# Kernel tuning notes

Hardware: AMD Instinct MI355X
Metric: run time of the kernel (lower is better)

## Reference

```python
import jax, jax.numpy as jnp
import numpy as np


def _conv3x3(x, w, b):
    # NCHW conv, stride 1, pad 1
    y = jax.lax.conv_general_dilated(x, w, (1, 1), ((1, 1), (1, 1)),
                                     dimension_numbers=('NCHW', 'OIHW', 'NCHW'))
    return y + b[None, :, None, None]


def _deform_conv3x3(x, offset, w):
    # Deformable conv v1: 3x3, stride 1, pad 1, 1 deformable group, no bias.
    # offset: [B, 18, H, W] laid out as (dy_k, dx_k) for k = 0..8 (row-major taps).
    B, C, H, W = x.shape
    K = 9
    off = offset.reshape(B, K, 2, H, W)
    ky, kx = jnp.meshgrid(jnp.arange(3), jnp.arange(3), indexing='ij')
    ky = (ky.reshape(K) - 1).astype(x.dtype)  # kernel tap y-offset, pad=1
    kx = (kx.reshape(K) - 1).astype(x.dtype)
    hh = jnp.arange(H, dtype=x.dtype)
    ww = jnp.arange(W, dtype=x.dtype)
    # sampling locations [B, K, H, W]
    sy = hh[None, None, :, None] + ky[None, :, None, None] + off[:, :, 0]
    sx = ww[None, None, None, :] + kx[None, :, None, None] + off[:, :, 1]
    y0 = jnp.floor(sy)
    x0 = jnp.floor(sx)
    ly = sy - y0  # fractional parts
    lx = sx - x0
    x_flat = x.reshape(B, C, H * W)

    def gather(yi, xi, wgt):
        # zero-padding semantics: corners outside the image contribute 0
        valid = (yi >= 0) & (yi < H) & (xi >= 0) & (xi < W)
        idx = (jnp.clip(yi, 0, H - 1).astype(jnp.int32) * W
               + jnp.clip(xi, 0, W - 1).astype(jnp.int32)).reshape(B, 1, K * H * W)
        v = jnp.take_along_axis(x_flat, idx, axis=2).reshape(B, C, K, H, W)
        return v * (wgt * valid.astype(x.dtype))[:, None]

    sampled = (gather(y0,     x0,     (1 - ly) * (1 - lx))
             + gather(y0,     x0 + 1, (1 - ly) * lx)
             + gather(y0 + 1, x0,     ly * (1 - lx))
             + gather(y0 + 1, x0 + 1, ly * lx))  # [B, C, K, H, W]
    return jnp.einsum('bckhw,ock->bohw', sampled, w.reshape(w.shape[0], C, K))


def setup_inputs() -> dict:
    key = jax.random.key(0)
    ks = jax.random.split(key, 8)
    C, O = 256, 256
    return {
        'kernel': jax.random.normal(ks[0], (16, C, 16, 16), jnp.float32),
        'search': jax.random.normal(ks[1], (16, C, 32, 32), jnp.float32),
        'Toffset_w': jax.random.normal(ks[2], (18, C, 3, 3), jnp.float32) * 0.02,
        'Toffset_b': jnp.zeros((18,), jnp.float32),
        'Tdeform_w': jax.random.normal(ks[3], (O, C, 3, 3), jnp.float32) * 0.02,
        'Soffset_w': jax.random.normal(ks[4], (18, C, 3, 3), jnp.float32) * 0.02,
        'Soffset_b': jnp.zeros((18,), jnp.float32),
        'Sdeform_w': jax.random.normal(ks[5], (O, C, 3, 3), jnp.float32) * 0.02,
    }


def reference(kernel, search, Toffset_w, Toffset_b, Tdeform_w,
              Soffset_w, Soffset_b, Sdeform_w):
    kernel_offset = _conv3x3(kernel, Toffset_w, Toffset_b)
    kernel_out = _deform_conv3x3(kernel, kernel_offset, Tdeform_w)
    search_offset = _conv3x3(search, Soffset_w, Soffset_b)
    search_out = _deform_conv3x3(search, search_offset, Sdeform_w)
    return (kernel_out, search_out, kernel_offset, search_offset)
```

## Files before the change

kernel.cpp:

```cpp
#include <hip/hip_runtime.h>

#define CIN   256
#define OC    256
#define K_TOT 2304
#define CCH   32
#define NCHK  8
#define KCH   288
#define SSTR  296
#define DM    64

#define N_DW  (OC * K_TOT)
#define N_OW  (32 * K_TOT)
#define N_CVT (2 * N_DW + 2 * N_OW)
#define CVT_BLOCKS (N_CVT / 4 / 256)

typedef short  bf16x8 __attribute__((ext_vector_type(8)));
typedef float  f32x4  __attribute__((ext_vector_type(4)));
typedef unsigned short ushort_t;

__device__ __forceinline__ ushort_t f2bf(float f) {
    unsigned u = __builtin_bit_cast(unsigned, f);
    u += 0x7fffu + ((u >> 16) & 1u);
    return (ushort_t)(u >> 16);
}
__device__ __forceinline__ float bf2f(short s) {
    return __builtin_bit_cast(float, ((unsigned)(unsigned short)s) << 16);
}

__global__ __launch_bounds__(256) void prep_k(
    const float* __restrict__ tdw, const float* __restrict__ sdw,
    const float* __restrict__ tow, const float* __restrict__ sow,
    const float* __restrict__ kin, const float* __restrict__ sin_,
    ushort_t* __restrict__ wk_d, ushort_t* __restrict__ ws_d,
    ushort_t* __restrict__ wk_o, ushort_t* __restrict__ ws_o,
    ushort_t* __restrict__ xt_k, ushort_t* __restrict__ xt_s)
{
    __shared__ ushort_t tile[64][264];

    if (blockIdx.x < CVT_BLOCKS) {
        const int i = (blockIdx.x * 256 + threadIdx.x) * 4;
        const float* src; ushort_t* dst; int j; bool offw = false;
        if (i < N_DW)                    { src = tdw; dst = wk_d; j = i; }
        else if (i < 2 * N_DW)           { src = sdw; dst = ws_d; j = i - N_DW; }
        else if (i < 2 * N_DW + N_OW)    { src = tow; dst = wk_o; j = i - 2 * N_DW; offw = true; }
        else                             { src = sow; dst = ws_o; j = i - 2 * N_DW - N_OW; offw = true; }
        const int oc = j / K_TOT;
        const int k  = j - oc * K_TOT;
        const int cc = k / KCH;
        const int r  = k - cc * KCH;
        const int tap = r >> 5;
        const int cl  = r & 31;
        ushort4 o4 = {0, 0, 0, 0};
        if (!offw || oc < 18) {
            const float* sp = &src[((size_t)oc * CIN + cc * 32 + cl) * 9 + tap];
            o4.x = f2bf(sp[0]); o4.y = f2bf(sp[9]); o4.z = f2bf(sp[18]); o4.w = f2bf(sp[27]);
        }
        *(ushort4*)&dst[j] = o4;
        return;
    }

    const int bx2 = blockIdx.x - CVT_BLOCKS;
    int H, W, b, px0; const float* x; ushort_t* xt;
    if (bx2 < 64) {
        H = 16; W = 16; x = kin; xt = xt_k;
        b = bx2 >> 2; px0 = (bx2 & 3) * 64;
    } else {
        int t2 = bx2 - 64;
        H = 32; W = 32; x = sin_; xt = xt_s;
        b = t2 >> 4; px0 = (t2 & 15) * 64;
    }
    const int HW = H * W;
    const int t = threadIdx.x, lane = t & 63, wv = t >> 6;
    const float* xb = x + (size_t)b * CIN * HW;

    for (int it = 0; it < 16; ++it) {
        const int ch = wv * 64 + it * 4 + (lane >> 4);
        const int pq = (lane & 15) * 4;
        float4 v = *(const float4*)&xb[(size_t)ch * HW + px0 + pq];
        tile[pq + 0][ch] = f2bf(v.x);
        tile[pq + 1][ch] = f2bf(v.y);
        tile[pq + 2][ch] = f2bf(v.z);
        tile[pq + 3][ch] = f2bf(v.w);
    }
    __syncthreads();
    for (int it = 0; it < 8; ++it) {
        const int px = it * 8 + wv * 2 + (lane >> 5);
        const int cg = (lane & 31) * 8;
        bf16x8 v = *(const bf16x8*)&tile[px][cg];
        *(bf16x8*)&xt[((size_t)b * HW + px0 + px) * 256 + cg] = v;
    }
}

__global__ __launch_bounds__(512, 2) void conv_gemm_k(
    const ushort_t* __restrict__ xt_k, const ushort_t* __restrict__ kwgt,
    const float* __restrict__ kbias, float* __restrict__ kout,
    const ushort_t* __restrict__ xt_s, const ushort_t* __restrict__ swgt,
    const float* __restrict__ sbias, float* __restrict__ sout)
{
    __shared__ float sred[3][4][2][64][4];

    int H, W, sh, b, px0;
    const ushort_t* xt; const ushort_t* wgt; const float* bias; float* out;
    if (blockIdx.x < 64) {
        H = 16; W = 16; sh = 4; xt = xt_k; wgt = kwgt; bias = kbias; out = kout;
        b = blockIdx.x >> 2; px0 = (blockIdx.x & 3) * 64;
    } else {
        int t2 = blockIdx.x - 64;
        H = 32; W = 32; sh = 5; xt = xt_s; wgt = swgt; bias = sbias; out = sout;
        b = t2 >> 4; px0 = (t2 & 15) * 64;
    }
    const int HW = H * W;
    const int t = threadIdx.x, lane = t & 63, wv = t >> 6;
    const int kh = wv >> 1;
    const int nt = wv & 1;
    const int l15 = lane & 15;
    const int cg8 = (lane >> 4) * 8;
    const ushort_t* xtb = xt + (size_t)b * HW * 256;

    int h[4], wc[4];
#pragma unroll
    for (int mt = 0; mt < 4; ++mt) {
        const int px = px0 + mt * 16 + l15;
        h[mt]  = px >> sh;
        wc[mt] = px & (W - 1);
    }
    const ushort_t* wrow = wgt + (size_t)(nt * 16 + l15) * K_TOT + cg8;

    f32x4 acc[4] = {};
    for (int cc = kh * 2; cc < kh * 2 + 2; ++cc) {
        const int cb = cc * 32 + cg8;
#pragma unroll
        for (int ks = 0; ks < 9; ++ks) {
            const bf16x8 b0 = *(const bf16x8*)&wrow[(size_t)cc * KCH + ks * 32];
            const int dy = ks / 3 - 1, dx = ks % 3 - 1;
#pragma unroll
            for (int mt = 0; mt < 4; ++mt) {
                const int y  = h[mt] + dy;
                const int xx = wc[mt] + dx;
                const bool ok = ((unsigned)y < (unsigned)H) && ((unsigned)xx < (unsigned)W);
                bf16x8 a = {};
                if (ok) a = *(const bf16x8*)&xtb[(size_t)(((y << sh) + xx) * 256 + cb)];
                acc[mt] = __builtin_amdgcn_mfma_f32_16x16x32_bf16(a, b0, acc[mt], 0, 0, 0);
            }
        }
    }

    if (kh > 0) {
#pragma unroll
        for (int mt = 0; mt < 4; ++mt)
            *(float4*)&sred[kh - 1][mt][nt][lane][0] = *(float4*)&acc[mt];
    }
    __syncthreads();
    if (kh == 0) {
        const int oc = nt * 16 + l15;
        const int prow = (lane >> 4) * 4;
        if (oc < 18) {
            const float bs = bias[oc];
#pragma unroll
            for (int mt = 0; mt < 4; ++mt) {
                float4 r = *(float4*)&acc[mt];
#pragma unroll
                for (int q = 0; q < 3; ++q) {
                    const float4 o = *(const float4*)&sred[q][mt][nt][lane][0];
                    r.x += o.x; r.y += o.y; r.z += o.z; r.w += o.w;
                }
                r.x += bs; r.y += bs; r.z += bs; r.w += bs;
                *(float4*)(out + ((size_t)b * 18 + oc) * HW + px0 + mt * 16 + prow) = r;
            }
        }
    }
}

__device__ __forceinline__ void dcn_load4(
    bf16x8* c, const ushort_t* __restrict__ xtb, int4 id, int cb)
{
    c[0] = *(const bf16x8*)&xtb[(size_t)id.x * 256 + cb];
    c[1] = *(const bf16x8*)&xtb[(size_t)id.y * 256 + cb];
    c[2] = *(const bf16x8*)&xtb[(size_t)id.z * 256 + cb];
    c[3] = *(const bf16x8*)&xtb[(size_t)id.w * 256 + cb];
}
__device__ __forceinline__ void dcn_proc2(
    ushort_t* swb, int so, const bf16x8* c, float4 wt)
{
    bf16x8 r;
#pragma unroll
    for (int j = 0; j < 8; ++j) {
        const float v = wt.x * bf2f(c[0][j]) + wt.y * bf2f(c[1][j])
                      + wt.z * bf2f(c[2][j]) + wt.w * bf2f(c[3][j]);
        r[j] = (short)f2bf(v);
    }
    *(bf16x8*)&swb[so] = r;
}

__global__ __launch_bounds__(512, 4) void deform_gemm_k(
    const ushort_t* __restrict__ xt_k, const float* __restrict__ koffs,
    const ushort_t* __restrict__ kwgt, float* __restrict__ kout,
    const ushort_t* __restrict__ xt_s, const float* __restrict__ soffs,
    const ushort_t* __restrict__ swgt_, float* __restrict__ sout)
{
    __shared__ __align__(16) ushort_t smp[DM][SSTR];
    __shared__ __align__(16) int      sidx[DM][9][4];
    __shared__ __align__(16) float    swt [DM][9][4];

    int H, W, b, px0;
    const ushort_t* xt; const float* offs; const ushort_t* wgt; float* out;
    if (blockIdx.x < 64) {
        const int xcd = blockIdx.x & 7, i = blockIdx.x >> 3;
        H = 16; W = 16; xt = xt_k; offs = koffs; wgt = kwgt; out = kout;
        b = xcd + 8 * (i & 1); px0 = (i >> 1) * 64;
    } else {
        const int t2 = blockIdx.x - 64;
        const int xcd = t2 & 7, i = t2 >> 3;
        H = 32; W = 32; xt = xt_s; offs = soffs; wgt = swgt_; out = sout;
        b = xcd + 8 * (i & 1); px0 = (i >> 1) * 64;
    }
    const int HW = H * W;
    const int t = threadIdx.x, lane = t & 63, wv = t >> 6;

#pragma unroll
    for (int u = 0; u < 2; ++u) {
        const int s = t + u * 512;
        if (s < DM * 9) {
            const int p = s / 9, k = s - 9 * p;
            const int pix = px0 + p;
            const int h  = pix / W;
            const int wc = pix - h * W;
            const float* ob = offs + (size_t)b * 18 * HW;
            const float dy = ob[(2 * k    ) * HW + pix];
            const float dx = ob[(2 * k + 1) * HW + pix];
            const float sy = (float)(h  + k / 3 - 1) + dy;
            const float sx = (float)(wc + k % 3 - 1) + dx;
            const float y0f = floorf(sy), x0f = floorf(sx);
            const float ly = sy - y0f, lx = sx - x0f;
            const int y0 = (int)y0f, x0 = (int)x0f;
#pragma unroll
            for (int j = 0; j < 4; ++j) {
                const int yy = y0 + (j >> 1);
                const int xx = x0 + (j & 1);
                const bool ok = ((unsigned)yy < (unsigned)H) && ((unsigned)xx < (unsigned)W);
                sidx[p][k][j] = min(max(yy, 0), H - 1) * W + min(max(xx, 0), W - 1);
                const float wj = ((j >> 1) ? ly : 1.f - ly) * ((j & 1) ? lx : 1.f - lx);
                swt[p][k][j] = ok ? wj : 0.f;
            }
        }
    }
    __syncthreads();

    const ushort_t* xtb = xt + (size_t)b * HW * 256;
    const int l15 = lane & 15;
    const int cg8 = (lane >> 4) * 8;
    const int ocb = wv * 32;
    const bool live4 = (t < 256);

    const int g0  = t >> 2;
    const int cgE = (t & 3) * 8;
    int uso[5];
#pragma unroll
    for (int q = 0; q < 5; ++q) {
        const int g  = g0 + q * 128;
        const int px = g / 9, tap = g - 9 * px;
        uso[q] = px * SSTR + tap * 32 + (t & 3) * 8;
    }

    const ushort_t* wrow0 = wgt + (size_t)(ocb      + l15) * K_TOT + cg8;
    const ushort_t* wrow1 = wgt + (size_t)(ocb + 16 + l15) * K_TOT + cg8;
    ushort_t* smpb = &smp[0][0];
    const int4*   sidxF = (const int4*)  &sidx[0][0][0];
    const float4* swtF  = (const float4*)&swt [0][0][0];

    f32x4 acc[4][2] = {};

    for (int cc = 0; cc < NCHK; ++cc) {
        const int cb = cc * 32 + cgE;
        const size_t kg0 = (size_t)cc * KCH;

        bf16x8 cA[4], cB[4];
        float4 wA, wB;
        bf16x8 bq[2][2];
        { const int4 id = sidxF[g0];       wA = swtF[g0];       dcn_load4(cA, xtb, id, cb); }
        { const int4 id = sidxF[g0 + 128]; wB = swtF[g0 + 128]; dcn_load4(cB, xtb, id, cb); }
        bq[0][0] = *(const bf16x8*)&wrow0[kg0];
        bq[0][1] = *(const bf16x8*)&wrow1[kg0];

        dcn_proc2(smpb, uso[0], cA, wA);
        { const int4 id = sidxF[g0 + 256]; wA = swtF[g0 + 256]; dcn_load4(cA, xtb, id, cb); }
        dcn_proc2(smpb, uso[1], cB, wB);
        { const int4 id = sidxF[g0 + 384]; wB = swtF[g0 + 384]; dcn_load4(cB, xtb, id, cb); }
        dcn_proc2(smpb, uso[2], cA, wA);
        if (live4) { const int4 id = sidxF[g0 + 512]; wA = swtF[g0 + 512]; dcn_load4(cA, xtb, id, cb); }
        dcn_proc2(smpb, uso[3], cB, wB);
        if (live4) dcn_proc2(smpb, uso[4], cA, wA);

        asm volatile("s_waitcnt lgkmcnt(0)" ::: "memory");
        __builtin_amdgcn_sched_barrier(0);
        __builtin_amdgcn_s_barrier();
        __builtin_amdgcn_sched_barrier(0);

        __builtin_amdgcn_s_setprio(1);
#pragma unroll
        for (int ks = 0; ks < 9; ++ks) {
            if (ks < 8) {
                bq[(ks + 1) & 1][0] = *(const bf16x8*)&wrow0[kg0 + (size_t)(ks + 1) * 32];
                bq[(ks + 1) & 1][1] = *(const bf16x8*)&wrow1[kg0 + (size_t)(ks + 1) * 32];
            }
            bf16x8 a[4];
#pragma unroll
            for (int mt = 0; mt < 4; ++mt)
                a[mt] = *(const bf16x8*)&smp[mt * 16 + l15][ks * 32 + cg8];
#pragma unroll
            for (int mt = 0; mt < 4; ++mt) {
                acc[mt][0] = __builtin_amdgcn_mfma_f32_16x16x32_bf16(a[mt], bq[ks & 1][0], acc[mt][0], 0, 0, 0);
                acc[mt][1] = __builtin_amdgcn_mfma_f32_16x16x32_bf16(a[mt], bq[ks & 1][1], acc[mt][1], 0, 0, 0);
            }
        }
        __builtin_amdgcn_s_setprio(0);

        if (cc < NCHK - 1) {
            __builtin_amdgcn_sched_barrier(0);
            __builtin_amdgcn_s_barrier();
            __builtin_amdgcn_sched_barrier(0);
        }
    }

    const int prow = (lane >> 4) * 4;
#pragma unroll
    for (int mt = 0; mt < 4; ++mt) {
#pragma unroll
        for (int nt = 0; nt < 2; ++nt) {
            const int oc = ocb + nt * 16 + l15;
            float* op = out + ((size_t)b * OC + oc) * HW + px0 + mt * 16 + prow;
            *(float4*)op = *(float4*)&acc[mt][nt];
        }
    }
}

extern "C" void kernel_launch(void* const* d_in, const int* in_sizes, int n_in,
                              void* d_out, int out_size, void* d_ws, size_t ws_size,
                              hipStream_t stream) {
    const float* kin = (const float*)d_in[0];
    const float* sin_ = (const float*)d_in[1];
    const float* tow = (const float*)d_in[2];
    const float* tob = (const float*)d_in[3];
    const float* tdw = (const float*)d_in[4];
    const float* sow = (const float*)d_in[5];
    const float* sob = (const float*)d_in[6];
    const float* sdw = (const float*)d_in[7];

    float* out = (float*)d_out;
    float* out_k  = out;
    float* out_s  = out_k + (size_t)16 * 256 * 16 * 16;
    float* out_ko = out_s + (size_t)16 * 256 * 32 * 32;
    float* out_so = out_ko + (size_t)16 * 18 * 16 * 16;

    ushort_t* wk_d = (ushort_t*)d_ws;
    ushort_t* ws_d = wk_d + N_DW;
    ushort_t* wk_o = ws_d + N_DW;
    ushort_t* ws_o = wk_o + N_OW;
    ushort_t* xt_k = ws_o + N_OW;
    ushort_t* xt_s = xt_k + (size_t)16 * 256 * 256;

    prep_k<<<dim3(CVT_BLOCKS + 320), 256, 0, stream>>>(
        tdw, sdw, tow, sow, kin, sin_,
        wk_d, ws_d, wk_o, ws_o, xt_k, xt_s);

    conv_gemm_k<<<dim3(320), 512, 0, stream>>>(
        xt_k, wk_o, tob, out_ko, xt_s, ws_o, sob, out_so);

    deform_gemm_k<<<dim3(320), 512, 0, stream>>>(
        xt_k, out_ko, wk_d, out_k, xt_s, out_so, ws_d, out_s);
}
```

Baseline: 222.0 us.

## Split offset-conv work across waves by pixel tile instead of K-chunks

Each wave in the offset-conv kernel now owns one 16-pixel M tile and loops over all 8 channel chunks, replacing the split-K scheme that needed an LDS reduction and a __syncthreads. Out-of-bounds taps use precomputed pointers to a zero row (assumed to be the zeroed padding rows of the offset weight buffer), so the inner loop carries no branches. Blocks are also remapped so consecutive block IDs spread batches across XCDs. The cost is more weight loads per wave and a dependence on that weight row being zero.

```diff
diff --git a/kernel.cpp b/kernel.cpp
--- a/kernel.cpp
+++ b/kernel.cpp
@@ -91,83 +91,64 @@
     }
 }
 
-__global__ __launch_bounds__(512, 2) void conv_gemm_k(
+__global__ __launch_bounds__(512) void conv_gemm_k(
     const ushort_t* __restrict__ xt_k, const ushort_t* __restrict__ kwgt,
     const float* __restrict__ kbias, float* __restrict__ kout,
     const ushort_t* __restrict__ xt_s, const ushort_t* __restrict__ swgt,
-    const float* __restrict__ sbias, float* __restrict__ sout)
-{
-    __shared__ float sred[3][4][2][64][4];
-
+    const float* __restrict__ sbias, float* __restrict__ sout,
+    const ushort_t* __restrict__ zp)
+{
     int H, W, sh, b, px0;
     const ushort_t* xt; const ushort_t* wgt; const float* bias; float* out;
     if (blockIdx.x < 64) {
+        const int xcd = blockIdx.x & 7, i = blockIdx.x >> 3;
         H = 16; W = 16; sh = 4; xt = xt_k; wgt = kwgt; bias = kbias; out = kout;
-        b = blockIdx.x >> 2; px0 = (blockIdx.x & 3) * 64;
+        b = xcd + 8 * (i & 1); px0 = (i >> 1) * 64;
     } else {
-        int t2 = blockIdx.x - 64;
+        const int t2 = blockIdx.x - 64;
+        const int xcd = t2 & 7, i = t2 >> 3;
         H = 32; W = 32; sh = 5; xt = xt_s; wgt = swgt; bias = sbias; out = sout;
-        b = t2 >> 4; px0 = (t2 & 15) * 64;
+        b = xcd + 8 * (i & 1); px0 = (i >> 1) * 64;
     }
     const int HW = H * W;
     const int t = threadIdx.x, lane = t & 63, wv = t >> 6;
-    const int kh = wv >> 1;
+    const int mt = wv >> 1;
     const int nt = wv & 1;
     const int l15 = lane & 15;
     const int cg8 = (lane >> 4) * 8;
     const ushort_t* xtb = xt + (size_t)b * HW * 256;
 
-    int h[4], wc[4];
-#pragma unroll
-    for (int mt = 0; mt < 4; ++mt) {
-        const int px = px0 + mt * 16 + l15;
-        h[mt]  = px >> sh;
-        wc[mt] = px & (W - 1);
+    const int px = px0 + mt * 16 + l15;
+    const int h  = px >> sh;
+    const int wc = px & (W - 1);
+
+    const ushort_t* pa[9];
+#pragma unroll
+    for (int ks = 0; ks < 9; ++ks) {
+        const int y  = h + ks / 3 - 1;
+        const int xx = wc + ks % 3 - 1;
+        const bool ok = ((unsigned)y < (unsigned)H) && ((unsigned)xx < (unsigned)W);
+        pa[ks] = ok ? (xtb + (size_t)(((y << sh) + xx) * 256 + cg8)) : zp;
     }
     const ushort_t* wrow = wgt + (size_t)(nt * 16 + l15) * K_TOT + cg8;
 
-    f32x4 acc[4] = {};
-    for (int cc = kh * 2; cc < kh * 2 + 2; ++cc) {
-        const int cb = cc * 32 + cg8;
+    f32x4 acc = {};
+#pragma unroll
+    for (int cc = 0; cc < NCHK; ++cc) {
 #pragma unroll
         for (int ks = 0; ks < 9; ++ks) {
+            const bf16x8 a  = *(const bf16x8*)&pa[ks][cc * 32];
             const bf16x8 b0 = *(const bf16x8*)&wrow[(size_t)cc * KCH + ks * 32];
-            const int dy = ks / 3 - 1, dx = ks % 3 - 1;
-#pragma unroll
-            for (int mt = 0; mt < 4; ++mt) {
-                const int y  = h[mt] + dy;
-                const int xx = wc[mt] + dx;
-                const bool ok = ((unsigned)y < (unsigned)H) && ((unsigned)xx < (unsigned)W);
-                bf16x8 a = {};
-                if (ok) a = *(const bf16x8*)&xtb[(size_t)(((y << sh) + xx) * 256 + cb)];
-                acc[mt] = __builtin_amdgcn_mfma_f32_16x16x32_bf16(a, b0, acc[mt], 0, 0, 0);
-            }
-        }
-    }
-
-    if (kh > 0) {
-#pragma unroll
-        for (int mt = 0; mt < 4; ++mt)
-            *(float4*)&sred[kh - 1][mt][nt][lane][0] = *(float4*)&acc[mt];
-    }
-    __syncthreads();
-    if (kh == 0) {
-        const int oc = nt * 16 + l15;
+            acc = __builtin_amdgcn_mfma_f32_16x16x32_bf16(a, b0, acc, 0, 0, 0);
+        }
+    }
+
+    const int oc = nt * 16 + l15;
+    if (oc < 18) {
+        const float bs = bias[oc];
         const int prow = (lane >> 4) * 4;
-        if (oc < 18) {
-            const float bs = bias[oc];
-#pragma unroll
-            for (int mt = 0; mt < 4; ++mt) {
-                float4 r = *(float4*)&acc[mt];
-#pragma unroll
-                for (int q = 0; q < 3; ++q) {
-                    const float4 o = *(const float4*)&sred[q][mt][nt][lane][0];
-                    r.x += o.x; r.y += o.y; r.z += o.z; r.w += o.w;
-                }
-                r.x += bs; r.y += bs; r.z += bs; r.w += bs;
-                *(float4*)(out + ((size_t)b * 18 + oc) * HW + px0 + mt * 16 + prow) = r;
-            }
-        }
+        float4 r = { acc.x + bs, acc.y + bs, acc.z + bs, acc.w + bs };
+        *(float4*)(out + ((size_t)b * 18 + oc) * HW + px0 + mt * 16 + prow) = r;
     }
 }
 
@@ -358,13 +339,14 @@
     ushort_t* ws_o = wk_o + N_OW;
     ushort_t* xt_k = ws_o + N_OW;
     ushort_t* xt_s = xt_k + (size_t)16 * 256 * 256;
+    const ushort_t* zp = wk_o + (size_t)31 * K_TOT;
 
     prep_k<<<dim3(CVT_BLOCKS + 320), 256, 0, stream>>>(
         tdw, sdw, tow, sow, kin, sin_,
         wk_d, ws_d, wk_o, ws_o, xt_k, xt_s);
 
     conv_gemm_k<<<dim3(320), 512, 0, stream>>>(
-        xt_k, wk_o, tob, out_ko, xt_s, ws_o, sob, out_so);
+        xt_k, wk_o, tob, out_ko, xt_s, ws_o, sob, out_so, zp);
 
     deform_gemm_k<<<dim3(320), 512, 0, stream>>>(
         xt_k, out_ko, wk_d, out_k, xt_s, out_so, ws_d, out_s);
```

New measurement: 245.6 us. 1.11x slower.
